# Performance work log

Hardware: AMD Instinct MI355X
Metric: run time of the kernel (lower is better)

Reference implementation:

```python
import jax, jax.numpy as jnp
import numpy as np

TEMPERATURE = 8.0  # sqrt(d_k=64)
MASK_FILL = -1e10  # -10000000000.0 in the original


def setup_inputs() -> dict:
    key = jax.random.key(0)
    kq, kk, kv, ke, km = jax.random.split(key, 5)
    B, Lq, Lk, D = 16, 2048, 2048, 64
    q = jax.random.normal(kq, (B, Lq, D), dtype=jnp.float32)
    k = jax.random.normal(kk, (B, Lk, D), dtype=jnp.float32)
    v = jax.random.normal(kv, (B, Lk, D), dtype=jnp.float32)
    explain_weight = jax.random.uniform(ke, (B, Lq, Lk), dtype=jnp.float32)
    mask = jax.random.randint(km, (B, Lq, Lk), 0, 2).astype(bool)
    return {"q": q, "k": k, "v": v, "explain_weight": explain_weight, "mask": mask}


def reference(q, k, v, explain_weight, mask):
    # attn = bmm(q, k^T) / temperature, masked fill, softmax over keys
    attn = jnp.einsum("bqd,bkd->bqk", q, k) / TEMPERATURE
    attn = jnp.where(mask, MASK_FILL, attn)
    attn = jax.nn.softmax(attn, axis=2)
    # dropout is identity in eval mode; post-softmax explain reweighting
    attn = attn * explain_weight
    output = jnp.einsum("bqk,bkd->bqd", attn, v)
    return (output, attn)
```

## Files before the change

kernel.cpp:

```cpp
#include <hip/hip_runtime.h>
#include <cstdint>
#include <cstddef>

#define NB 16
#define NL 2048
#define ND 64
#define QT 16
#define NW 8
#define NTHREADS (NW * 64)
#define SLICE (NL / NW)
#define NT (SLICE / 16)
#define ROWU 1026
#define ELSU (QT * ROWU)
#define LDSB (ELSU * 4)

typedef __attribute__((ext_vector_type(8))) short bf16x8;
typedef __attribute__((ext_vector_type(4))) float f32x4;
typedef __attribute__((ext_vector_type(4))) int i32x4;
typedef __attribute__((ext_vector_type(4))) unsigned short u16x4;
typedef __attribute__((ext_vector_type(2))) unsigned int u32x2;
typedef __attribute__((ext_vector_type(4))) unsigned int u32x4;
typedef unsigned short u16;

#define MFMA __builtin_amdgcn_mfma_f32_16x16x32_bf16

__device__ __forceinline__ u16 f2bf(float x) {
  union { float f; uint32_t u; } v; v.f = x;
  uint32_t r = v.u + 0x7FFFu + ((v.u >> 16) & 1u);
  return (u16)(r >> 16);
}
__device__ __forceinline__ float bfhi2f(uint32_t w) {
  union { uint32_t u; float f; } v; v.u = w & 0xFFFF0000u; return v.f;
}
__device__ __forceinline__ float bflo2f(uint32_t w) {
  union { uint32_t u; float f; } v; v.u = w << 16; return v.f;
}
__device__ __forceinline__ int swzb(int cb) { return cb ^ (((cb >> 7) & 7) << 4); }

template <int MODE>
__device__ __forceinline__ uint32_t mnib(const void* __restrict__ m, size_t i) {
  if constexpr (MODE == 1) {
    const uint32_t x = __builtin_nontemporal_load((const uint32_t*)((const uint8_t*)m + i));
    return (x | (x >> 7) | (x >> 14) | (x >> 21)) & 0xFu;
  } else if constexpr (MODE == 0) {
    const i32x4 x = __builtin_nontemporal_load(((const i32x4*)((const int*)m + i)));
    return (uint32_t)(x[0] != 0) | ((uint32_t)(x[1] != 0) << 1) |
           ((uint32_t)(x[2] != 0) << 2) | ((uint32_t)(x[3] != 0) << 3);
  } else if constexpr (MODE == 2) {
    const f32x4 x = __builtin_nontemporal_load(((const f32x4*)((const float*)m + i)));
    return (uint32_t)(x[0] != 0.f) | ((uint32_t)(x[1] != 0.f) << 1) |
           ((uint32_t)(x[2] != 0.f) << 2) | ((uint32_t)(x[3] != 0.f) << 3);
  } else {
    const uint32_t* p = (const uint32_t*)m + 2 * i;
    return (uint32_t)(p[0] != 0u) | ((uint32_t)(p[2] != 0u) << 1) |
           ((uint32_t)(p[4] != 0u) << 2) | ((uint32_t)(p[6] != 0u) << 3);
  }
}

template <bool WS>
__device__ __forceinline__ void loadKfrag(const float* __restrict__ k,
                                          const u16* __restrict__ kb,
                                          int b, int row, int kg,
                                          bf16x8& b0, bf16x8& b1) {
  if constexpr (WS) {
    const u16* kp = kb + ((size_t)(b * NL + row)) * ND + kg * 8;
    b0 = *(const bf16x8*)kp;
    b1 = *(const bf16x8*)(kp + 32);
  } else {
    const float* kp = k + ((size_t)(b * NL + row)) * ND + kg * 8;
#pragma unroll
    for (int i = 0; i < 8; ++i) {
      b0[i] = (short)f2bf(kp[i]);
      b1[i] = (short)f2bf(kp[i + 32]);
    }
  }
}

template <int MMODE, bool WS>
__device__ __forceinline__ void attn_core(
    const float* __restrict__ q, const float* __restrict__ k,
    const float* __restrict__ v, const float* __restrict__ ew,
    const void* __restrict__ mask,
    const u16* __restrict__ qs, const u16* __restrict__ kb,
    const u16* __restrict__ vt, const uint32_t* __restrict__ mb,
    float* __restrict__ out, float* __restrict__ attn,
    uint32_t* __restrict__ els, float* __restrict__ rsums) {
  const int tid = threadIdx.x;
  const int lane = tid & 63;
  const int w = tid >> 6;
  const int fr = lane & 15;
  const int kg = lane >> 4;

  const int bid = blockIdx.x;
  const int swzid = (bid & 7) * ((NB * (NL / QT)) / 8) + (bid >> 3);
  const int b = swzid >> 7;
  const int q0 = (swzid & 127) * QT;
  const int cbase = w * SLICE;
  const size_t bq = (size_t)b * NL + q0;
  const size_t mrow0 = bq * NL;
  const size_t lrow = mrow0 + (size_t)fr * NL + (size_t)(cbase + 4 * kg);

  const float* ewbase = ew + bq * NL + cbase + 4 * lane;
  f32x4 ewr[16];
#pragma unroll
  for (int r = 0; r < 16; ++r)
    ewr[r] = __builtin_nontemporal_load((const f32x4*)(ewbase + (size_t)r * NL));

  bf16x8 a0, a1;
  if constexpr (WS) {
    const u16* qp = qs + (bq + fr) * ND + kg * 8;
    a0 = *(const bf16x8*)qp;
    a1 = *(const bf16x8*)(qp + 32);
  } else {
    const float* qp = q + (bq + fr) * ND + kg * 8;
#pragma unroll
    for (int i = 0; i < 8; ++i) {
      a0[i] = (short)f2bf(qp[i] * 0.125f);
      a1[i] = (short)f2bf(qp[i + 32] * 0.125f);
    }
  }

  uint32_t mw[8];
  if constexpr (WS) {
    const uint32_t* mbr = mb + (bq + fr) * (NL / 32) + (cbase >> 5);
#pragma unroll
    for (int u = 0; u < 8; ++u) mw[u] = mbr[u];
  }

  float rs = 0.f;
#pragma unroll
  for (int ti = 0; ti < NT; ++ti) {
    const int c0 = cbase + ti * 16;
    bf16x8 b0, b1;
    loadKfrag<WS>(k, kb, b, c0 + fr, kg, b0, b1);
    f32x4 s = {0.f, 0.f, 0.f, 0.f};
    s = MFMA(b0, a0, s, 0, 0, 0);
    s = MFMA(b1, a1, s, 0, 0, 0);
    uint32_t nib;
    if constexpr (WS) nib = (mw[ti >> 1] >> (16 * (ti & 1) + 4 * kg)) & 0xFu;
    else              nib = mnib<MMODE>(mask, lrow + (size_t)(ti * 16));
    const float e0 = (nib & 1u) ? 0.f : __expf(s[0]);
    const float e1 = (nib & 2u) ? 0.f : __expf(s[1]);
    const float e2 = (nib & 4u) ? 0.f : __expf(s[2]);
    const float e3 = (nib & 8u) ? 0.f : __expf(s[3]);
    rs += (e0 + e1) + (e2 + e3);
    u32x2 ep;
    ep[0] = (uint32_t)f2bf(e0) | ((uint32_t)f2bf(e1) << 16);
    ep[1] = (uint32_t)f2bf(e2) | ((uint32_t)f2bf(e3) << 16);
    *(u32x2*)(els + fr * ROWU + (swzb((c0 + 4 * kg) * 2) >> 2)) = ep;
  }
  rs += __shfl_xor(rs, 16, 64);
  rs += __shfl_xor(rs, 32, 64);
  if (lane < 16) rsums[w * QT + fr] = rs;

#pragma unroll
  for (int r = 0; r < 16; ++r) asm volatile("" : "+v"(ewr[r]));
  __syncthreads();

  float invf = 0.f;
#pragma unroll
  for (int ww = 0; ww < NW; ++ww) invf += rsums[ww * QT + fr];
  invf = 1.0f / invf;

  float* atb = attn + bq * NL + cbase + 4 * lane;
  const int lofs = swzb((cbase + 4 * lane) * 2) >> 2;
#pragma unroll
  for (int r = 0; r < 16; ++r) {
    const u32x2 el = *(const u32x2*)(els + r * ROWU + lofs);
    const float inv_r = __shfl(invf, r, 64);
    f32x4 p;
    p[0] = bflo2f(el[0]) * inv_r * ewr[r][0];
    p[1] = bfhi2f(el[0]) * inv_r * ewr[r][1];
    p[2] = bflo2f(el[1]) * inv_r * ewr[r][2];
    p[3] = bfhi2f(el[1]) * inv_r * ewr[r][3];
    __builtin_nontemporal_store(p, (f32x4*)(atb + (size_t)r * NL));
    u32x2 pp;
    pp[0] = (uint32_t)f2bf(p[0]) | ((uint32_t)f2bf(p[1]) << 16);
    pp[1] = (uint32_t)f2bf(p[2]) | ((uint32_t)f2bf(p[3]) << 16);
    *(u32x2*)(els + r * ROWU + lofs) = pp;
  }

  f32x4 oA[4] = {{0.f,0.f,0.f,0.f},{0.f,0.f,0.f,0.f},{0.f,0.f,0.f,0.f},{0.f,0.f,0.f,0.f}};
#pragma unroll
  for (int gi = 0; gi < NT / 2; ++gi) {
    union { u32x4 u; bf16x8 v8; } pu;
    pu.u = *(const u32x4*)(els + fr * ROWU + (swzb((cbase + 32 * gi + 8 * kg) * 2) >> 2));
    const bf16x8 pa = pu.v8;
    const int kk = cbase + gi * 32 + kg * 8;
    if constexpr (WS) {
      const u16* vp = vt + ((size_t)(b * ND + fr)) * NL + kk;
      oA[0] = MFMA(pa, *(const bf16x8*)(vp),           oA[0], 0, 0, 0);
      oA[1] = MFMA(pa, *(const bf16x8*)(vp + 16 * NL), oA[1], 0, 0, 0);
      oA[2] = MFMA(pa, *(const bf16x8*)(vp + 32 * NL), oA[2], 0, 0, 0);
      oA[3] = MFMA(pa, *(const bf16x8*)(vp + 48 * NL), oA[3], 0, 0, 0);
    } else {
#pragma unroll
      for (int dt = 0; dt < 4; ++dt) {
        bf16x8 vf;
#pragma unroll
        for (int i = 0; i < 8; ++i)
          vf[i] = (short)f2bf(v[((size_t)(b * NL + kk + i)) * ND + dt * 16 + fr]);
        oA[dt] = MFMA(pa, vf, oA[dt], 0, 0, 0);
      }
    }
  }
  __syncthreads();

  float* osta = (float*)els;
  f32x4 acc = {0.f, 0.f, 0.f, 0.f};
  const int rrr = tid >> 4;
  const int d4 = (tid & 15) * 4;
#pragma unroll
  for (int round = 0; round < NW / 2; ++round) {
    if ((w >> 1) == round) {
      float* od = osta + (w & 1) * (QT * ND);
#pragma unroll
      for (int dt = 0; dt < 4; ++dt)
#pragma unroll
        for (int j = 0; j < 4; ++j)
          od[(4 * kg + j) * ND + dt * 16 + fr] = oA[dt][j];
    }
    __syncthreads();
    if (tid < QT * ND / 4) {
      acc += *(const f32x4*)(osta + rrr * ND + d4) +
             *(const f32x4*)(osta + QT * ND + rrr * ND + d4);
    }
    __syncthreads();
  }
  if (tid < QT * ND / 4)
    *(f32x4*)(out + (bq + rrr) * ND + d4) = acc;
}

__global__ void __launch_bounds__(NTHREADS, 4)
attn_ws(const float* __restrict__ q, const float* __restrict__ k,
        const float* __restrict__ v, const float* __restrict__ ew,
        const u16* __restrict__ qs, const u16* __restrict__ kb,
        const u16* __restrict__ vt, const uint32_t* __restrict__ mb,
        float* __restrict__ out, float* __restrict__ attn) {
  extern __shared__ uint32_t els[];
  __shared__ float rsums[NW * QT];
  attn_core<0, true>(q, k, v, ew, nullptr, qs, kb, vt, mb, out, attn, els, rsums);
}

__global__ void __launch_bounds__(NTHREADS, 4)
attn_fb(const float* __restrict__ q, const float* __restrict__ k,
        const float* __restrict__ v, const float* __restrict__ ew,
        const void* __restrict__ mask,
        float* __restrict__ out, float* __restrict__ attn) {
  extern __shared__ uint32_t els[];
  __shared__ float rsums[NW * QT];
  __shared__ int s_mode;
  if (threadIdx.x < 64) {
    const uint32_t x = ((const uint32_t*)mask)[threadIdx.x];
    const int all01 = __all(x <= 1u);
    const int allf  = __all(x == 0u || x == 0x3F800000u);
    const int oddz  = __all(((threadIdx.x & 1) == 0) || (x == 0u));
    if (threadIdx.x == 0) s_mode = all01 ? (oddz ? 3 : 0) : (allf ? 2 : 1);
  }
  __syncthreads();
  switch (s_mode) {
    case 0:  attn_core<0, false>(q, k, v, ew, mask, nullptr, nullptr, nullptr, nullptr, out, attn, els, rsums); break;
    case 1:  attn_core<1, false>(q, k, v, ew, mask, nullptr, nullptr, nullptr, nullptr, out, attn, els, rsums); break;
    case 2:  attn_core<2, false>(q, k, v, ew, mask, nullptr, nullptr, nullptr, nullptr, out, attn, els, rsums); break;
    default: attn_core<3, false>(q, k, v, ew, mask, nullptr, nullptr, nullptr, nullptr, out, attn, els, rsums); break;
  }
}

__global__ void __launch_bounds__(256)
prep_qk(const float* __restrict__ q, const float* __restrict__ k,
        u16* __restrict__ qs, u16* __restrict__ kb) {
  const size_t NQ4 = (size_t)NB * NL * ND / 4;
  const size_t i = (size_t)blockIdx.x * 256 + threadIdx.x;
  f32x4 val;
  u16* dst;
  if (i < NQ4) {
    val = ((const f32x4*)q)[i];
    val *= 0.125f;
    dst = qs + i * 4;
  } else {
    val = ((const f32x4*)k)[i - NQ4];
    dst = kb + (i - NQ4) * 4;
  }
  u16x4 o;
#pragma unroll
  for (int j = 0; j < 4; ++j) o[j] = f2bf(val[j]);
  *(u16x4*)dst = o;
}

__global__ void __launch_bounds__(256)
prep_vt(const float* __restrict__ v, u16* __restrict__ vt) {
  __shared__ float t[64 * 68];
  const int b = blockIdx.y;
  const int k0 = blockIdx.x * 64;
  const int tid = threadIdx.x;
  const int rr = tid >> 4;
  const int c4 = (tid & 15) * 4;
#pragma unroll
  for (int i = 0; i < 4; ++i) {
    const int r = rr + 16 * i;
    const f32x4 val = *(const f32x4*)(v + ((size_t)(b * NL + k0 + r)) * ND + c4);
    *(f32x4*)(t + r * 68 + c4) = val;
  }
  __syncthreads();
#pragma unroll
  for (int i = 0; i < 4; ++i) {
    const int d = rr + 16 * i;
    u16x4 o;
#pragma unroll
    for (int j = 0; j < 4; ++j) o[j] = f2bf(t[(c4 + j) * 68 + d]);
    *(u16x4*)(vt + ((size_t)(b * ND + d)) * NL + k0 + c4) = o;
  }
}

__global__ void __launch_bounds__(256)
prep_mask(const void* __restrict__ mask, uint32_t* __restrict__ mb) {
  __shared__ int pm;
  if (threadIdx.x < 64) {
    const uint32_t x = ((const uint32_t*)mask)[threadIdx.x];
    const int all01 = __all(x <= 1u);
    const int allf  = __all(x == 0u || x == 0x3F800000u);
    const int oddz  = __all(((threadIdx.x & 1) == 0) || (x == 0u));
    if (threadIdx.x == 0) pm = all01 ? (oddz ? 3 : 0) : (allf ? 2 : 1);
  }
  __syncthreads();
  const int mode = pm;
  const size_t t = (size_t)blockIdx.x * 256 + threadIdx.x;
  uint32_t bits = 0;
  if (mode == 1) {
    const u32x4 x0 = *(((const u32x4*)mask) + t * 2);
    const u32x4 x1 = *(((const u32x4*)mask) + t * 2 + 1);
#pragma unroll
    for (int i = 0; i < 4; ++i)
#pragma unroll
      for (int by = 0; by < 4; ++by) {
        bits |= (((x0[i] >> (8 * by)) & 0xFFu) ? 1u : 0u) << (i * 4 + by);
        bits |= (((x1[i] >> (8 * by)) & 0xFFu) ? 1u : 0u) << (16 + i * 4 + by);
      }
  } else if (mode == 0 || mode == 2) {
#pragma unroll
    for (int c = 0; c < 8; ++c) {
      const u32x4 x = *(((const u32x4*)mask) + t * 8 + c);
#pragma unroll
      for (int i = 0; i < 4; ++i) bits |= (x[i] ? 1u : 0u) << (c * 4 + i);
    }
  } else {
    const uint32_t* p = (const uint32_t*)mask;
#pragma unroll
    for (int i = 0; i < 32; ++i) bits |= (p[2 * (t * 32 + i)] ? 1u : 0u) << i;
  }
  mb[t] = bits;
}

extern "C" void kernel_launch(void* const* d_in, const int* in_sizes, int n_in,
                              void* d_out, int out_size, void* d_ws, size_t ws_size,
                              hipStream_t stream) {
  const float* q    = (const float*)d_in[0];
  const float* k    = (const float*)d_in[1];
  const float* v    = (const float*)d_in[2];
  const float* ew   = (const float*)d_in[3];
  const void*  mask = d_in[4];
  float* out  = (float*)d_out;
  float* attn = out + (size_t)NB * NL * ND;

  const size_t QE = (size_t)NB * NL * ND;
  const size_t MBW = (size_t)NB * NL * (NL / 32);
  u16* qs = (u16*)d_ws;
  u16* kb = qs + QE;
  u16* vt = kb + QE;
  uint32_t* mb = (uint32_t*)(vt + QE);

  (void)hipFuncSetAttribute(reinterpret_cast<const void*>(attn_ws),
                            hipFuncAttributeMaxDynamicSharedMemorySize, LDSB);
  (void)hipFuncSetAttribute(reinterpret_cast<const void*>(attn_fb),
                            hipFuncAttributeMaxDynamicSharedMemorySize, LDSB);

  dim3 grid(NB * (NL / QT));
  if (ws_size >= 3 * QE * sizeof(u16) + MBW * sizeof(uint32_t)) {
    prep_qk<<<dim3((unsigned)(2 * QE / 4 / 256)), 256, 0, stream>>>(q, k, qs, kb);
    prep_vt<<<dim3(NL / 64, NB), 256, 0, stream>>>(v, vt);
    prep_mask<<<dim3((unsigned)(MBW / 256)), 256, 0, stream>>>(mask, mb);
    attn_ws<<<grid, NTHREADS, LDSB, stream>>>(q, k, v, ew, qs, kb, vt, mb, out, attn);
  } else {
    attn_fb<<<grid, NTHREADS, LDSB, stream>>>(q, k, v, ew, mask, out, attn);
  }
}
```

Baseline: 249.4 us.

## Halve query tile to 8 rows and raise occupancy with late explain-weight loads

Shrinks the per-block query tile from 16 to 8 rows. Each 16x16 MFMA tile now duplicates rows (fr&7), so half of the QK^T and PV compute is redundant. The explain_weight loads move out of the register-prefetch array into the normalization loop, which frees VGPRs and lets launch bounds request 8 blocks per SM instead of 4. LDS per block halves and the grid doubles. The cost is wasted MFMA work, K/V fragments reloaded twice as often across blocks, and ew loads no longer overlapped with the QK phase. Nontemporal loads and stores are also replaced with normal ones.

Result: slower. 469.1 us (+88.1%).

```diff
diff --git a/kernel.cpp b/kernel.cpp
--- a/kernel.cpp
+++ b/kernel.cpp
@@ -5,7 +5,7 @@
 #define NB 16
 #define NL 2048
 #define ND 64
-#define QT 16
+#define QT 8
 #define NW 8
 #define NTHREADS (NW * 64)
 #define SLICE (NL / NW)
@@ -13,6 +13,7 @@
 #define ROWU 1026
 #define ELSU (QT * ROWU)
 #define LDSB (ELSU * 4)
+#define OSR 16
 
 typedef __attribute__((ext_vector_type(8))) short bf16x8;
 typedef __attribute__((ext_vector_type(4))) float f32x4;
@@ -90,29 +91,23 @@
   const int w = tid >> 6;
   const int fr = lane & 15;
   const int kg = lane >> 4;
+  const int frq = fr & 7;
 
   const int bid = blockIdx.x;
   const int swzid = (bid & 7) * ((NB * (NL / QT)) / 8) + (bid >> 3);
-  const int b = swzid >> 7;
-  const int q0 = (swzid & 127) * QT;
+  const int b = swzid >> 8;
+  const int q0 = (swzid & 255) * QT;
   const int cbase = w * SLICE;
   const size_t bq = (size_t)b * NL + q0;
-  const size_t mrow0 = bq * NL;
-  const size_t lrow = mrow0 + (size_t)fr * NL + (size_t)(cbase + 4 * kg);
-
-  const float* ewbase = ew + bq * NL + cbase + 4 * lane;
-  f32x4 ewr[16];
-#pragma unroll
-  for (int r = 0; r < 16; ++r)
-    ewr[r] = __builtin_nontemporal_load((const f32x4*)(ewbase + (size_t)r * NL));
+  const size_t lrow = bq * NL + (size_t)frq * NL + (size_t)(cbase + 4 * kg);
 
   bf16x8 a0, a1;
   if constexpr (WS) {
-    const u16* qp = qs + (bq + fr) * ND + kg * 8;
+    const u16* qp = qs + (bq + frq) * ND + kg * 8;
     a0 = *(const bf16x8*)qp;
     a1 = *(const bf16x8*)(qp + 32);
   } else {
-    const float* qp = q + (bq + fr) * ND + kg * 8;
+    const float* qp = q + (bq + frq) * ND + kg * 8;
 #pragma unroll
     for (int i = 0; i < 8; ++i) {
       a0[i] = (short)f2bf(qp[i] * 0.125f);
@@ -122,7 +117,7 @@
 
   uint32_t mw[8];
   if constexpr (WS) {
-    const uint32_t* mbr = mb + (bq + fr) * (NL / 32) + (cbase >> 5);
+    const uint32_t* mbr = mb + (bq + frq) * (NL / 32) + (cbase >> 5);
 #pragma unroll
     for (int u = 0; u < 8; ++u) mw[u] = mbr[u];
   }
@@ -144,36 +139,37 @@
     const float e2 = (nib & 4u) ? 0.f : __expf(s[2]);
     const float e3 = (nib & 8u) ? 0.f : __expf(s[3]);
     rs += (e0 + e1) + (e2 + e3);
-    u32x2 ep;
-    ep[0] = (uint32_t)f2bf(e0) | ((uint32_t)f2bf(e1) << 16);
-    ep[1] = (uint32_t)f2bf(e2) | ((uint32_t)f2bf(e3) << 16);
-    *(u32x2*)(els + fr * ROWU + (swzb((c0 + 4 * kg) * 2) >> 2)) = ep;
+    if (fr < 8) {
+      u32x2 ep;
+      ep[0] = (uint32_t)f2bf(e0) | ((uint32_t)f2bf(e1) << 16);
+      ep[1] = (uint32_t)f2bf(e2) | ((uint32_t)f2bf(e3) << 16);
+      *(u32x2*)(els + fr * ROWU + (swzb((c0 + 4 * kg) * 2) >> 2)) = ep;
+    }
   }
   rs += __shfl_xor(rs, 16, 64);
   rs += __shfl_xor(rs, 32, 64);
-  if (lane < 16) rsums[w * QT + fr] = rs;
-
-#pragma unroll
-  for (int r = 0; r < 16; ++r) asm volatile("" : "+v"(ewr[r]));
+  if (lane < 8) rsums[w * QT + lane] = rs;
   __syncthreads();
 
   float invf = 0.f;
 #pragma unroll
-  for (int ww = 0; ww < NW; ++ww) invf += rsums[ww * QT + fr];
+  for (int ww = 0; ww < NW; ++ww) invf += rsums[ww * QT + frq];
   invf = 1.0f / invf;
 
+  const float* ewb = ew + bq * NL + cbase + 4 * lane;
   float* atb = attn + bq * NL + cbase + 4 * lane;
   const int lofs = swzb((cbase + 4 * lane) * 2) >> 2;
 #pragma unroll
-  for (int r = 0; r < 16; ++r) {
+  for (int r = 0; r < QT; ++r) {
+    const f32x4 w4 = *(const f32x4*)(ewb + (size_t)r * NL);
     const u32x2 el = *(const u32x2*)(els + r * ROWU + lofs);
     const float inv_r = __shfl(invf, r, 64);
     f32x4 p;
-    p[0] = bflo2f(el[0]) * inv_r * ewr[r][0];
-    p[1] = bfhi2f(el[0]) * inv_r * ewr[r][1];
-    p[2] = bflo2f(el[1]) * inv_r * ewr[r][2];
-    p[3] = bfhi2f(el[1]) * inv_r * ewr[r][3];
-    __builtin_nontemporal_store(p, (f32x4*)(atb + (size_t)r * NL));
+    p[0] = bflo2f(el[0]) * inv_r * w4[0];
+    p[1] = bfhi2f(el[0]) * inv_r * w4[1];
+    p[2] = bflo2f(el[1]) * inv_r * w4[2];
+    p[3] = bfhi2f(el[1]) * inv_r * w4[3];
+    *(f32x4*)(atb + (size_t)r * NL) = p;
     u32x2 pp;
     pp[0] = (uint32_t)f2bf(p[0]) | ((uint32_t)f2bf(p[1]) << 16);
     pp[1] = (uint32_t)f2bf(p[2]) | ((uint32_t)f2bf(p[3]) << 16);
@@ -184,7 +180,7 @@
 #pragma unroll
   for (int gi = 0; gi < NT / 2; ++gi) {
     union { u32x4 u; bf16x8 v8; } pu;
-    pu.u = *(const u32x4*)(els + fr * ROWU + (swzb((cbase + 32 * gi + 8 * kg) * 2) >> 2));
+    pu.u = *(const u32x4*)(els + frq * ROWU + (swzb((cbase + 32 * gi + 8 * kg) * 2) >> 2));
     const bf16x8 pa = pu.v8;
     const int kk = cbase + gi * 32 + kg * 8;
     if constexpr (WS) {
@@ -213,7 +209,7 @@
 #pragma unroll
   for (int round = 0; round < NW / 2; ++round) {
     if ((w >> 1) == round) {
-      float* od = osta + (w & 1) * (QT * ND);
+      float* od = osta + (w & 1) * (OSR * ND);
 #pragma unroll
       for (int dt = 0; dt < 4; ++dt)
 #pragma unroll
@@ -223,7 +219,7 @@
     __syncthreads();
     if (tid < QT * ND / 4) {
       acc += *(const f32x4*)(osta + rrr * ND + d4) +
-             *(const f32x4*)(osta + QT * ND + rrr * ND + d4);
+             *(const f32x4*)(osta + OSR * ND + rrr * ND + d4);
     }
     __syncthreads();
   }
@@ -231,7 +227,7 @@
     *(f32x4*)(out + (bq + rrr) * ND + d4) = acc;
 }
 
-__global__ void __launch_bounds__(NTHREADS, 4)
+__global__ void __launch_bounds__(NTHREADS, 8)
 attn_ws(const float* __restrict__ q, const float* __restrict__ k,
         const float* __restrict__ v, const float* __restrict__ ew,
         const u16* __restrict__ qs, const u16* __restrict__ kb,
```
